# Performance work log

Measured on AMD Instinct MI355X. Metric: run time of the kernel, lower is better.

The kernel has to match this reference:

```python
import jax, jax.numpy as jnp
from jax import lax
import numpy as np

N, C, T, V, P, O = 32, 64, 300, 25, 3, 128
STRIDE = 2
EPS = 1e-5


def setup_inputs() -> dict:
    key = jax.random.key(0)
    ks = jax.random.split(key, 8)
    x = jax.random.normal(ks[0], (N, C, T, V), jnp.float32)
    A_parts = jax.random.uniform(ks[1], (P, V, V), jnp.float32)
    edge_importance = jnp.ones((P,), jnp.float32)
    gcn_w = jax.random.normal(ks[2], (O, C), jnp.float32) * 0.05
    gcn_b = jax.random.normal(ks[3], (O,), jnp.float32) * 0.05
    tcn_w = jax.random.normal(ks[4], (O, O, 9, 1), jnp.float32) * 0.02
    tcn_b = jax.random.normal(ks[5], (O,), jnp.float32) * 0.05
    bn_gamma = jnp.ones((O,), jnp.float32)
    bn_beta = jnp.zeros((O,), jnp.float32)
    res_w = jax.random.normal(ks[6], (O, C), jnp.float32) * 0.05
    res_b = jax.random.normal(ks[7], (O,), jnp.float32) * 0.05
    return {"x": x, "A_parts": A_parts, "edge_importance": edge_importance,
            "gcn_w": gcn_w, "gcn_b": gcn_b, "tcn_w": tcn_w, "tcn_b": tcn_b,
            "bn_gamma": bn_gamma, "bn_beta": bn_beta, "res_w": res_w, "res_b": res_b}


def reference(x, A_parts, edge_importance, gcn_w, gcn_b, tcn_w, tcn_b,
              bn_gamma, bn_beta, res_w, res_b):
    # Fused P-partition aggregation: sum_p (ei_p * A_p) applied once.
    A_sum = jnp.einsum('pvw,p->vw', A_parts, edge_importance)  # [V, V]
    agg = jnp.einsum('nctv,vw->nctw', x, A_sum)                # [N, C, T, V]
    # 1x1 gcn conv == channel matmul
    x_gcn = jnp.einsum('nctv,oc->notv', agg, gcn_w) + gcn_b[None, :, None, None]
    # temporal conv: kernel (9,1), stride (2,1), pad (4,0)
    x_tcn = lax.conv_general_dilated(
        x_gcn, tcn_w, window_strides=(STRIDE, 1), padding=((4, 4), (0, 0)),
        dimension_numbers=('NCHW', 'OIHW', 'NCHW'))
    x_tcn = x_tcn + tcn_b[None, :, None, None]
    # BatchNorm (training mode: batch statistics, biased variance)
    mean = jnp.mean(x_tcn, axis=(0, 2, 3), keepdims=True)
    var = jnp.var(x_tcn, axis=(0, 2, 3), keepdims=True)
    x_bn = (x_tcn - mean) * lax.rsqrt(var + EPS)
    x_bn = x_bn * bn_gamma[None, :, None, None] + bn_beta[None, :, None, None]
    # residual: 1x1 conv, stride (2,1) == temporal subsample + channel matmul
    x_sub = x[:, :, ::STRIDE, :]
    res = jnp.einsum('nctv,oc->notv', x_sub, res_w) + res_b[None, :, None, None]
    return jax.nn.relu(x_bn + res)
```

## Files before the change

kernel.cpp:

```cpp
#include <hip/hip_runtime.h>
#include <hip/hip_bf16.h>

typedef unsigned short u16;
typedef unsigned int   u32;

#define NB 32
#define CC 64
#define TT 300
#define VV 25
#define OO 128
#define TO 150
#define KT 9
#define MM 7500
#define MT 59
#define M2 3750

typedef short s8v  __attribute__((ext_vector_type(8)));
typedef float f4v  __attribute__((ext_vector_type(4)));
typedef u16  h4v  __attribute__((ext_vector_type(4)));
typedef u16  h8v  __attribute__((ext_vector_type(8)));

__device__ __forceinline__ float b2f(u16 u){
  union { u32 i; float f; } c; c.i = ((u32)u) << 16; return c.f;
}
__device__ __forceinline__ u16 f2b(float f){
  __hip_bfloat16 h = __float2bfloat16(f);
  return *reinterpret_cast<u16*>(&h);
}
__device__ __forceinline__ void async16(const void* g, void* l){
  __builtin_amdgcn_global_load_lds((const __attribute__((address_space(1))) u32*)g,
                                   (__attribute__((address_space(3))) u32*)l, 16, 0, 0);
}

__global__ __launch_bounds__(256) void k_prep(const float* __restrict__ Ap, const float* __restrict__ ei,
                                              const float* __restrict__ tw, const float* __restrict__ gw,
                                              const float* __restrict__ rw,
                                              float* __restrict__ Asum, float* __restrict__ zbuf,
                                              u16* __restrict__ Wq2, u16* __restrict__ gwb,
                                              u16* __restrict__ rwb){
  int idx = blockIdx.x * 256 + threadIdx.x;
  if (idx < VV*VV){
    float s = 0.f;
    for (int p = 0; p < 3; ++p) s += ei[p] * Ap[p*VV*VV + idx];
    Asum[idx] = s;
  }
  if (idx >= 640 && idx < 768) zbuf[idx - 640] = 0.f;
  int w = idx - 1024;
  if (w >= 0 && w < 18*OO*64){
    int kc = w >> 13;
    int r  = w & 8191;
    int o  = r >> 6;
    int j  = r & 63;
    int k  = kc >> 1;
    int i  = (kc & 1)*64 + j;
    Wq2[w] = f2b(tw[o*(OO*KT) + i*KT + k]);
  }
  int w2 = idx - 148480;
  if (w2 >= 0 && w2 < OO*CC) gwb[w2] = f2b(gw[w2]);
  int w3 = idx - 156672;
  if (w3 >= 0 && w3 < OO*CC) rwb[w3] = f2b(rw[w3]);
}

__global__ __launch_bounds__(256, 4) void k_gcnm(const float* __restrict__ x, const float* __restrict__ Asum,
                                                 const u16* __restrict__ gwb, const float* __restrict__ gb,
                                                 u16* __restrict__ xg){
  __shared__ __align__(16) u16 A_lds[128*64];
  __shared__ __align__(16) u16 B_lds[128*64];
  int bx = blockIdx.x;
  int n  = bx / MT;
  int m0 = (bx % MT) * 128;
  int t0 = m0 / VV, r0 = m0 % VV;
  int tid = threadIdx.x;
  int lane = tid & 63, wv = tid >> 6;
  int wm = (wv & 1) * 64, wo = (wv >> 1) * 64;
  int lr = lane & 15, lq = lane >> 4;

  {
    const char* gB = (const char*)gwb;
    char* lB = (char*)B_lds;
    #pragma unroll
    for (int i = 0; i < 4; ++i){
      int G = i*256 + tid;
      int row = G >> 3, gp = G & 7;
      int src = (row*8 + (gp ^ (row & 7)))*16;
      async16(gB + src, lB + G*16);
    }
  }

  s8v bfw[2];
  #pragma unroll
  for (int wt = 0; wt < 2; ++wt){
    u16 tmp[8];
    int w = lr + 16*wt;
    #pragma unroll
    for (int j = 0; j < 8; ++j){
      int v = lq*8 + j;
      tmp[j] = (w < VV && v < VV) ? f2b(Asum[v*VV + w]) : (u16)0;
    }
    bfw[wt] = *(s8v*)tmp;
  }

  asm volatile("s_waitcnt vmcnt(0)" ::: "memory");
  __builtin_amdgcn_sched_barrier(0);

  const size_t XTOT = (size_t)NB*CC*TT*VV;
  f4v xa7[7], xb7[7];
  #pragma unroll
  for (int tt = 0; tt < 7; ++tt){
    int tau = tt*4 + wv;
    int it = tau >> 2, ct = tau & 3;
    int t  = t0 + it;
    int c  = ct*16 + lr;
    size_t off = ((size_t)(n*CC + c)*TT + t)*VV + lq*8;
    if (lq == 3) off -= 7;
    if (off > XTOT - 8) off = XTOT - 8;
    const float* xp = x + off;
    asm volatile("global_load_dwordx4 %0, %1, off"            : "=&v"(xa7[tt]) : "v"(xp));
    asm volatile("global_load_dwordx4 %0, %1, off offset:16"  : "=&v"(xb7[tt]) : "v"(xp));
  }

  #pragma unroll
  for (int tt = 0; tt < 7; ++tt){
    if      (tt == 0) asm volatile("s_waitcnt vmcnt(12)" ::: "memory");
    else if (tt == 1) asm volatile("s_waitcnt vmcnt(10)" ::: "memory");
    else if (tt == 2) asm volatile("s_waitcnt vmcnt(8)"  ::: "memory");
    else if (tt == 3) asm volatile("s_waitcnt vmcnt(6)"  ::: "memory");
    else if (tt == 4) asm volatile("s_waitcnt vmcnt(4)"  ::: "memory");
    else if (tt == 5) asm volatile("s_waitcnt vmcnt(2)"  ::: "memory");
    else              asm volatile("s_waitcnt vmcnt(0)"  ::: "memory");
    __builtin_amdgcn_sched_barrier(0);

    int tau = tt*4 + wv;
    int it = tau >> 2, ct = tau & 3;
    int t  = t0 + it;
    bool valid = (t < TT);
    u16 pk[8];
    if (lq < 3){
      if (valid){
        pk[0]=f2b(xa7[tt][0]); pk[1]=f2b(xa7[tt][1]); pk[2]=f2b(xa7[tt][2]); pk[3]=f2b(xa7[tt][3]);
        pk[4]=f2b(xb7[tt][0]); pk[5]=f2b(xb7[tt][1]); pk[6]=f2b(xb7[tt][2]); pk[7]=f2b(xb7[tt][3]);
      } else {
        #pragma unroll
        for (int j = 0; j < 8; ++j) pk[j] = 0;
      }
    } else {
      pk[0] = valid ? f2b(xb7[tt][3]) : (u16)0;
      pk[1]=0; pk[2]=0; pk[3]=0; pk[4]=0; pk[5]=0; pk[6]=0; pk[7]=0;
    }
    s8v af = *(s8v*)pk;
    f4v d0 = (f4v)(0.f), d1 = (f4v)(0.f);
    d0 = __builtin_amdgcn_mfma_f32_16x16x32_bf16(af, bfw[0], d0, 0, 0, 0);
    d1 = __builtin_amdgcn_mfma_f32_16x16x32_bf16(af, bfw[1], d1, 0, 0, 0);
    int cb = ct*16 + lq*4;
    int g  = cb >> 3, co = cb & 7;
    int ml0 = it*VV + lr - r0;
    if (ml0 >= 0 && ml0 < 128){
      u16 q[4];
      #pragma unroll
      for (int rg = 0; rg < 4; ++rg) q[rg] = f2b(d0[rg]);
      *(h4v*)&A_lds[ml0*64 + ((g ^ (ml0 & 7))*8) + co] = *(h4v*)q;
    }
    int w1 = lr + 16;
    int ml1 = it*VV + w1 - r0;
    if (w1 < VV && ml1 >= 0 && ml1 < 128){
      u16 q[4];
      #pragma unroll
      for (int rg = 0; rg < 4; ++rg) q[rg] = f2b(d1[rg]);
      *(h4v*)&A_lds[ml1*64 + ((g ^ (ml1 & 7))*8) + co] = *(h4v*)q;
    }
  }
  __syncthreads();

  f4v acc[4][4];
  #pragma unroll
  for (int mi = 0; mi < 4; ++mi)
    #pragma unroll
    for (int ni = 0; ni < 4; ++ni) acc[mi][ni] = (f4v)(0.f);
  #pragma unroll
  for (int ks = 0; ks < 2; ++ks){
    int p = ((ks*4 + lq) ^ (lane & 7)) * 8;
    s8v af[4], bf[4];
    #pragma unroll
    for (int mi = 0; mi < 4; ++mi)
      af[mi] = *(const s8v*)&A_lds[(wm + mi*16 + lr)*64 + p];
    #pragma unroll
    for (int ni = 0; ni < 4; ++ni)
      bf[ni] = *(const s8v*)&B_lds[(wo + ni*16 + lr)*64 + p];
    #pragma unroll
    for (int mi = 0; mi < 4; ++mi)
      #pragma unroll
      for (int ni = 0; ni < 4; ++ni)
        acc[mi][ni] = __builtin_amdgcn_mfma_f32_16x16x32_bf16(af[mi], bf[ni], acc[mi][ni], 0, 0, 0);
  }

  float bias[4];
  #pragma unroll
  for (int ni = 0; ni < 4; ++ni) bias[ni] = gb[wo + ni*16 + lr];
  #pragma unroll
  for (int mi = 0; mi < 4; ++mi){
    int mr = m0 + wm + mi*16 + lq*4;
    #pragma unroll
    for (int ni = 0; ni < 4; ++ni){
      int o = wo + ni*16 + lr;
      #pragma unroll
      for (int rg = 0; rg < 4; ++rg){
        int m = mr + rg;
        if (m < MM)
          xg[((size_t)n*MM + m)*OO + o] = f2b(acc[mi][ni][rg] + bias[ni]);
      }
    }
  }
}

#define TCN_ISSUE(KC, SET) do {                                                         \
    const u16* wbase_ = Wq2 + (KC)*8192;                                                \
    char* Bb_ = (char*)(&B_lds[SET][0]);                                                \
    async16(wbase_ + (0*64 + rlow)*64 + gsrc*8, Bb_ + 0*8192 + tid16);                  \
    async16(wbase_ + (1*64 + rlow)*64 + gsrc*8, Bb_ + 1*8192 + tid16);                  \
    _Pragma("unroll")                                                                   \
    for (int mi_ = 0; mi_ < 2; ++mi_){                                                  \
      int t_ = tb_[mi_] + ((KC) >> 1);                                                  \
      bool val_ = mv_[mi_] && (t_ >= 0) && (t_ < TT);                                   \
      const u16* p_ = val_ ? (xgn + (size_t)(t_*VV + vv_[mi_])*OO + ((KC)&1)*64 + jo)   \
                           : (zbuf + jo);                                               \
      asm volatile("global_load_dwordx4 %0, %1, off"           : "=&v"(aR[SET][mi_*2+0]) : "v"(p_)); \
      asm volatile("global_load_dwordx4 %0, %1, off offset:64" : "=&v"(aR[SET][mi_*2+1]) : "v"(p_)); \
    }                                                                                   \
  } while(0)

__global__ __launch_bounds__(512, 4) void k_tcnm(const u16* __restrict__ xg, const u16* __restrict__ Wq2,
                                                 const float* __restrict__ tb, const u16* __restrict__ zbuf,
                                                 u16* __restrict__ xt, float* __restrict__ psum,
                                                 float* __restrict__ psq){
  __shared__ __align__(16) u16 B_lds[2][128*64];
  __shared__ float sredS[8][64];
  __shared__ float sredQ[8][64];
  int bx = blockIdx.x;
  int lg = ((bx & 7) * 120) + (bx >> 3);
  int n  = lg / 30;
  int m0 = (lg % 30) * 128;
  int tid = threadIdx.x;
  int lane = tid & 63, wv = tid >> 6;
  int wm = (wv >> 1) * 32, wo = (wv & 1) * 64;
  int lr = lane & 15, lq = lane >> 4;

  int rlow = tid >> 3;
  int gsrc = (tid & 7) ^ (rlow & 7);
  int tid16 = tid * 16;

  int tb_[2], vv_[2]; bool mv_[2];
  #pragma unroll
  for (int mi = 0; mi < 2; ++mi){
    int m_ = m0 + wm + mi*16 + lr;
    mv_[mi] = (m_ < M2);
    int t2 = m_ / VV, v = m_ - t2*VV;
    tb_[mi] = 2*t2 - 4;
    vv_[mi] = v;
  }
  const u16* xgn = xg + (size_t)n*MM*OO;
  int jo = lq*8;

  f4v acc[2][4];
  #pragma unroll
  for (int mi = 0; mi < 2; ++mi)
    #pragma unroll
    for (int ni = 0; ni < 4; ++ni) acc[mi][ni] = (f4v)(0.f);

  s8v aR[2][4];

  TCN_ISSUE(0, 0);

  #pragma unroll
  for (int kc = 0; kc < 18; ++kc){
    asm volatile("s_waitcnt vmcnt(0)" ::: "memory");
    __builtin_amdgcn_sched_barrier(0);
    __builtin_amdgcn_s_barrier();
    asm volatile("" ::: "memory");

    if (kc < 17){
      if ((kc & 1) == 0) TCN_ISSUE(kc+1, 1);
      else               TCN_ISSUE(kc+1, 0);
    }

    const u16* Bc = &B_lds[kc & 1][0];
    #pragma unroll
    for (int ks = 0; ks < 2; ++ks){
      int p = ((ks*4 + lq) ^ (lane & 7)) * 8;
      s8v bf[4];
      #pragma unroll
      for (int ni = 0; ni < 4; ++ni)
        bf[ni] = *(const s8v*)&Bc[(wo + ni*16 + lr)*64 + p];
      #pragma unroll
      for (int mi = 0; mi < 2; ++mi)
        #pragma unroll
        for (int ni = 0; ni < 4; ++ni)
          acc[mi][ni] = __builtin_amdgcn_mfma_f32_16x16x32_bf16(aR[kc & 1][mi*2+ks], bf[ni], acc[mi][ni], 0, 0, 0);
    }
    asm volatile("s_waitcnt lgkmcnt(0)" ::: "memory");
    __builtin_amdgcn_s_barrier();
    asm volatile("" ::: "memory");
  }

  float bias[4];
  #pragma unroll
  for (int ni = 0; ni < 4; ++ni) bias[ni] = tb[wo + ni*16 + lr];
  float sni[4] = {0.f,0.f,0.f,0.f}, qni[4] = {0.f,0.f,0.f,0.f};
  #pragma unroll
  for (int mi = 0; mi < 2; ++mi){
    int mr = m0 + wm + mi*16 + lq*4;
    #pragma unroll
    for (int ni = 0; ni < 4; ++ni){
      int o = wo + ni*16 + lr;
      #pragma unroll
      for (int rg = 0; rg < 4; ++rg){
        int mm = mr + rg;
        if (mm < M2){
          float val = acc[mi][ni][rg] + bias[ni];
          xt[((size_t)n*M2 + mm)*OO + o] = f2b(val);
          sni[ni] += val;
          qni[ni] += val*val;
        }
      }
    }
  }
  #pragma unroll
  for (int ni = 0; ni < 4; ++ni){
    float s = sni[ni], q = qni[ni];
    s += __shfl_xor(s, 16); s += __shfl_xor(s, 32);
    q += __shfl_xor(q, 16); q += __shfl_xor(q, 32);
    if (lane < 16){
      sredS[wv][ni*16 + lane] = s;
      sredQ[wv][ni*16 + lane] = q;
    }
  }
  __syncthreads();
  if (tid < 128){
    int o = tid, h = o >> 6, lo = o & 63;
    psum[(size_t)lg*128 + o] = (sredS[h][lo] + sredS[h+2][lo]) + (sredS[h+4][lo] + sredS[h+6][lo]);
  } else if (tid < 256){
    int o = tid - 128, h = o >> 6, lo = o & 63;
    psq [(size_t)lg*128 + o] = (sredQ[h][lo] + sredQ[h+2][lo]) + (sredQ[h+4][lo] + sredQ[h+6][lo]);
  }
}

__global__ __launch_bounds__(256) void k_stats2a(const float* __restrict__ psum, const float* __restrict__ psq,
                                                 float* __restrict__ ps2, float* __restrict__ pq2){
  __shared__ float bufS[256], bufQ[256];
  int tid = threadIdx.x, b = blockIdx.x;
  int o = tid & 127, h = tid >> 7;
  float s = 0.f, q = 0.f;
  for (int r = b*16 + h; r < b*16 + 16; r += 2){
    s += psum[(size_t)r*128 + o];
    q += psq [(size_t)r*128 + o];
  }
  bufS[tid] = s; bufQ[tid] = q;
  __syncthreads();
  if (tid < 128){
    ps2[(size_t)b*128 + o] = bufS[tid] + bufS[tid + 128];
    pq2[(size_t)b*128 + o] = bufQ[tid] + bufQ[tid + 128];
  }
}

__global__ __launch_bounds__(256) void k_stats2b(const float* __restrict__ ps2, const float* __restrict__ pq2,
                                                 const float* __restrict__ gamma, const float* __restrict__ beta,
                                                 float* __restrict__ stats){
  __shared__ float bufS[256], bufQ[256];
  int tid = threadIdx.x;
  int o = tid & 127, h = tid >> 7;
  float s = 0.f, q = 0.f;
  for (int b = h; b < 60; b += 2){
    s += ps2[(size_t)b*128 + o];
    q += pq2[(size_t)b*128 + o];
  }
  bufS[tid] = s; bufQ[tid] = q;
  __syncthreads();
  if (tid < 128){
    s = bufS[tid] + bufS[tid + 128];
    q = bufQ[tid] + bufQ[tid + 128];
    const float inv = 1.f / 120000.f;
    float mean = s * inv;
    float var  = q * inv - mean*mean;
    float sc = gamma[o] * rsqrtf(var + 1e-5f);
    stats[o]       = sc;
    stats[128 + o] = beta[o] - mean * sc;
  }
}

__global__ __launch_bounds__(256, 4) void k_resm(const float* __restrict__ x, const u16* __restrict__ rwb,
                                                 const float* __restrict__ rb, const u16* __restrict__ xt,
                                                 const float* __restrict__ stats, float* __restrict__ out){
  __shared__ __align__(16) char smem[64*130*4];
  u16* A_lds = (u16*)smem;
  u16* B_lds = A_lds + 128*64;
  float* tbuf = (float*)smem;
  int bx = blockIdx.x;
  int n  = bx / 30;
  int m0 = (bx % 30) * 128;
  int t20 = m0 / VV, r0 = m0 % VV;
  int tid = threadIdx.x;
  int lane = tid & 63, wv = tid >> 6;
  int wm = (wv & 1) * 64, wo = (wv >> 1) * 64;
  int lr = lane & 15, lq = lane >> 4;

  {
    const u32* g32 = (const u32*)rwb;
    u32* b32 = (u32*)B_lds;
    for (int s = tid; s < 4096; s += 256){
      int row = s >> 5, col = s & 31;
      int g = col >> 2, c2 = col & 3;
      b32[row*32 + ((g ^ (row & 7))*4 + c2)] = g32[s];
    }
  }

  for (int task = tid; task < 8*7*VV; task += 256){
    int cg  = task / (7*VV);
    int rem = task - cg*(7*VV);
    int t2i = rem / VV, v = rem - t2i*VV;
    int t2 = t20 + t2i;
    int ml = t2i*VV + v - r0;
    if (ml >= 0 && ml < 128){
      u16 pk[8];
      if (t2 < TO){
        const float* xp = x + ((size_t)(n*CC + cg*8)*TT + 2*t2)*VV + v;
        #pragma unroll
        for (int cc = 0; cc < 8; ++cc) pk[cc] = f2b(xp[(size_t)cc*(TT*VV)]);
      } else {
        #pragma unroll
        for (int cc = 0; cc < 8; ++cc) pk[cc] = 0;
      }
      *(h8v*)&A_lds[ml*64 + ((cg ^ (ml & 7))*8)] = *(h8v*)pk;
    }
  }
  __syncthreads();

  f4v acc[4][4];
  #pragma unroll
  for (int mi = 0; mi < 4; ++mi)
    #pragma unroll
    for (int ni = 0; ni < 4; ++ni) acc[mi][ni] = (f4v)(0.f);
  #pragma unroll
  for (int ks = 0; ks < 2; ++ks){
    int p = ((ks*4 + lq) ^ (lane & 7)) * 8;
    s8v af[4], bf[4];
    #pragma unroll
    for (int mi = 0; mi < 4; ++mi)
      af[mi] = *(const s8v*)&A_lds[(wm + mi*16 + lr)*64 + p];
    #pragma unroll
    for (int ni = 0; ni < 4; ++ni)
      bf[ni] = *(const s8v*)&B_lds[(wo + ni*16 + lr)*64 + p];
    #pragma unroll
    for (int mi = 0; mi < 4; ++mi)
      #pragma unroll
      for (int ni = 0; ni < 4; ++ni)
        acc[mi][ni] = __builtin_amdgcn_mfma_f32_16x16x32_bf16(af[mi], bf[ni], acc[mi][ni], 0, 0, 0);
  }

  float sc[4], sb[4], rr[4];
  #pragma unroll
  for (int ni = 0; ni < 4; ++ni){
    int o = wo + ni*16 + lr;
    sc[ni] = stats[o]; sb[ni] = stats[128 + o]; rr[ni] = rb[o];
  }

  #pragma unroll
  for (int pass = 0; pass < 2; ++pass){
    __syncthreads();
    if ((wv >> 1) == pass){
      #pragma unroll
      for (int mi = 0; mi < 4; ++mi){
        int mb   = m0 + wm + mi*16 + lq*4;
        int mloc = wm + mi*16 + lq*4;
        #pragma unroll
        for (int ni = 0; ni < 4; ++ni){
          int o    = wo + ni*16 + lr;
          int oloc = ni*16 + lr;
          size_t xb = ((size_t)n*M2 + mb)*OO + o;
          float v2[4];
          #pragma unroll
          for (int rg = 0; rg < 4; ++rg){
            float val = 0.f;
            if (mb + rg < M2)
              val = fmaxf(sc[ni]*b2f(xt[xb + (size_t)rg*OO]) + sb[ni] + acc[mi][ni][rg] + rr[ni], 0.f);
            v2[rg] = val;
          }
          *(float2*)&tbuf[oloc*130 + mloc]     = make_float2(v2[0], v2[1]);
          *(float2*)&tbuf[oloc*130 + mloc + 2] = make_float2(v2[2], v2[3]);
        }
      }
    }
    __syncthreads();
    #pragma unroll
    for (int it = 0; it < 16; ++it){
      int row = it*4 + (tid >> 6);
      int c2  = (tid & 63) * 2;
      int o   = pass*64 + row;
      int mg  = m0 + c2;
      size_t ob = ((size_t)(n*OO + o))*M2 + mg;
      float2 vv = *(float2*)&tbuf[row*130 + c2];
      if (mg + 1 < M2)      *(float2*)&out[ob] = vv;
      else if (mg < M2)     out[ob] = vv.x;
    }
  }
}

extern "C" void kernel_launch(void* const* d_in, const int* in_sizes, int n_in,
                              void* d_out, int out_size, void* d_ws, size_t ws_size,
                              hipStream_t stream) {
  const float* x     = (const float*)d_in[0];
  const float* Ap    = (const float*)d_in[1];
  const float* ei    = (const float*)d_in[2];
  const float* gw    = (const float*)d_in[3];
  const float* gb    = (const float*)d_in[4];
  const float* tw    = (const float*)d_in[5];
  const float* tb    = (const float*)d_in[6];
  const float* gamma = (const float*)d_in[7];
  const float* beta  = (const float*)d_in[8];
  const float* rw    = (const float*)d_in[9];
  const float* rb    = (const float*)d_in[10];
  float* out = (float*)d_out;

  char* ws = (char*)d_ws;
  float* Asum  = (float*)ws;
  float* zbuf  = (float*)(ws + 2560);
  u16*   Wq2   = (u16*)(ws + 4096);
  u16*   gwb   = (u16*)(ws + 299008);
  u16*   rwb   = (u16*)(ws + 315392);
  float* stats = (float*)(ws + 331776);
  float* psum  = (float*)(ws + 333824);
  float* psq   = (float*)(ws + 825344);
  float* ps2   = (float*)(ws + 1316864);
  float* pq2   = (float*)(ws + 1347584);
  u16*   xg    = (u16*)(ws + (2u<<20));
  u16*   xt    = (u16*)(ws + 63537152);

  k_prep   <<<dim3(644),    dim3(256), 0, stream>>>(Ap, ei, tw, gw, rw, Asum, zbuf, Wq2, gwb, rwb);
  k_gcnm   <<<dim3(NB*MT),  dim3(256), 0, stream>>>(x, Asum, gwb, gb, xg);
  k_tcnm   <<<dim3(NB*30),  dim3(512), 0, stream>>>(xg, Wq2, tb, (const u16*)zbuf, xt, psum, psq);
  k_stats2a<<<dim3(60),     dim3(256), 0, stream>>>(psum, psq, ps2, pq2);
  k_stats2b<<<dim3(1),      dim3(256), 0, stream>>>(ps2, pq2, gamma, beta, stats);
  k_resm   <<<dim3(NB*30),  dim3(256), 0, stream>>>(x, rwb, rb, xt, stats, out);
}
```

Measured before the change: 293.7 us.

## Issue next tcn chunk loads before waiting, using partial vmcnt waits

The temporal-conv main loop is restructured into a two-stage ping-pong. The loads for chunk k+1 are issued before waiting on chunk k, and the wait only drains down to vmcnt(6), so the next chunk's global loads and async weight copies stay in flight during the current MFMA work. Before, every iteration drained all outstanding loads with vmcnt(0) before computing. The loop is no longer fully unrolled, and correctness relies on the exact count of outstanding memory operations matching the vmcnt value.

```diff
diff --git a/kernel.cpp b/kernel.cpp
--- a/kernel.cpp
+++ b/kernel.cpp
@@ -228,6 +228,30 @@
     }                                                                                   \
   } while(0)
 
+#define TCN_COMPUTE(SET) do {                                                           \
+    const u16* Bc_ = &B_lds[SET][0];                                                    \
+    _Pragma("unroll")                                                                   \
+    for (int ks_ = 0; ks_ < 2; ++ks_){                                                  \
+      int p_ = ((ks_*4 + lq) ^ (lane & 7)) * 8;                                         \
+      s8v bf_[4];                                                                       \
+      _Pragma("unroll")                                                                 \
+      for (int ni_ = 0; ni_ < 4; ++ni_)                                                 \
+        bf_[ni_] = *(const s8v*)&Bc_[(wo + ni_*16 + lr)*64 + p_];                       \
+      _Pragma("unroll")                                                                 \
+      for (int mi_ = 0; mi_ < 2; ++mi_)                                                 \
+        _Pragma("unroll")                                                               \
+        for (int ni_ = 0; ni_ < 4; ++ni_)                                               \
+          acc[mi_][ni_] = __builtin_amdgcn_mfma_f32_16x16x32_bf16(aR[SET][mi_*2+ks_], bf_[ni_], acc[mi_][ni_], 0, 0, 0); \
+    }                                                                                   \
+  } while(0)
+
+#define TCN_BAR_IN()  do { __builtin_amdgcn_sched_barrier(0);                           \
+                           __builtin_amdgcn_s_barrier();                                \
+                           asm volatile("" ::: "memory"); } while(0)
+#define TCN_BAR_OUT() do { asm volatile("s_waitcnt lgkmcnt(0)" ::: "memory");           \
+                           __builtin_amdgcn_s_barrier();                                \
+                           asm volatile("" ::: "memory"); } while(0)
+
 __global__ __launch_bounds__(512, 4) void k_tcnm(const u16* __restrict__ xg, const u16* __restrict__ Wq2,
                                                  const float* __restrict__ tb, const u16* __restrict__ zbuf,
                                                  u16* __restrict__ xt, float* __restrict__ psum,
@@ -270,35 +294,22 @@
 
   TCN_ISSUE(0, 0);
 
-  #pragma unroll
-  for (int kc = 0; kc < 18; ++kc){
-    asm volatile("s_waitcnt vmcnt(0)" ::: "memory");
-    __builtin_amdgcn_sched_barrier(0);
-    __builtin_amdgcn_s_barrier();
-    asm volatile("" ::: "memory");
-
-    if (kc < 17){
-      if ((kc & 1) == 0) TCN_ISSUE(kc+1, 1);
-      else               TCN_ISSUE(kc+1, 0);
-    }
-
-    const u16* Bc = &B_lds[kc & 1][0];
-    #pragma unroll
-    for (int ks = 0; ks < 2; ++ks){
-      int p = ((ks*4 + lq) ^ (lane & 7)) * 8;
-      s8v bf[4];
-      #pragma unroll
-      for (int ni = 0; ni < 4; ++ni)
-        bf[ni] = *(const s8v*)&Bc[(wo + ni*16 + lr)*64 + p];
-      #pragma unroll
-      for (int mi = 0; mi < 2; ++mi)
-        #pragma unroll
-        for (int ni = 0; ni < 4; ++ni)
-          acc[mi][ni] = __builtin_amdgcn_mfma_f32_16x16x32_bf16(aR[kc & 1][mi*2+ks], bf[ni], acc[mi][ni], 0, 0, 0);
-    }
-    asm volatile("s_waitcnt lgkmcnt(0)" ::: "memory");
-    __builtin_amdgcn_s_barrier();
-    asm volatile("" ::: "memory");
+  for (int kc2 = 0; kc2 < 9; ++kc2){
+    int kc = kc2*2;
+    TCN_ISSUE(kc+1, 1);
+    asm volatile("s_waitcnt vmcnt(6)" ::: "memory");
+    TCN_BAR_IN();
+    TCN_COMPUTE(0);
+    TCN_BAR_OUT();
+    if (kc2 < 8){
+      TCN_ISSUE(kc+2, 0);
+      asm volatile("s_waitcnt vmcnt(6)" ::: "memory");
+    } else {
+      asm volatile("s_waitcnt vmcnt(0)" ::: "memory");
+    }
+    TCN_BAR_IN();
+    TCN_COMPUTE(1);
+    TCN_BAR_OUT();
   }
 
   float bias[4];
```

After: 296.8 us. Within noise of the previous version (+1.1%).
